# Performance work log

Measured on AMD Instinct MI355X. Metric: run time of the kernel, lower is better.

Reference implementation:

```python
import jax, jax.numpy as jnp
import numpy as np

SEQ_LEN, BATCH, N_FEATURES, CONTEXT = 2048, 32, 1024, 20


def setup_inputs() -> dict:
    key = jax.random.key(0)
    k1, k2 = jax.random.split(key)
    x = jax.random.normal(k1, (SEQ_LEN, BATCH, N_FEATURES), dtype=jnp.float32)
    stdv = 1.0 / np.sqrt(CONTEXT + 1)
    weight = jax.random.uniform(
        k2, (N_FEATURES, CONTEXT + 1), dtype=jnp.float32, minval=-stdv, maxval=stdv
    )
    return {"x": x, "weight": weight}


def reference(x, weight):
    # x: (S, B, F); weight: (F, C+1)
    # y[t, b, f] = sum_{c=0}^{C} x[t+c, b, f] * weight[f, c], zero-padded past t=S-1.
    S, B, F = x.shape
    C = weight.shape[1] - 1
    lhs = jnp.transpose(x, (1, 2, 0))          # (B, F, S)  NCW layout
    rhs = weight[:, None, :]                   # (F, 1, C+1) depthwise kernel
    out = jax.lax.conv_general_dilated(
        lhs, rhs,
        window_strides=(1,),
        padding=[(0, C)],                      # causal lookahead: pad right only
        feature_group_count=F,
    )                                          # (B, F, S) cross-correlation == torch math
    return jnp.transpose(out, (2, 0, 1))       # (S, B, F)
```

## Files before the change

### kernel.cpp

```cpp
#include <hip/hip_runtime.h>

#define S_LEN   2048
#define BATCH   32
#define NF      1024
#define CTX     20
#define KW      21
#define T_OUT   256
#define F_TILE  32
#define NCHUNK  36
#define BUF_FLOATS (NCHUNK * 8 * F_TILE)
#define R_PER_T 8
#define T_WIN   (R_PER_T + CTX)
#define N_TILES (S_LEN / T_OUT)

#define WAITV(n) asm volatile("s_waitcnt vmcnt(" #n ")" ::: "memory")

typedef float f32x4_t __attribute__((ext_vector_type(4)));

__device__ __forceinline__ void stage_tile(const float* __restrict__ x,
                                           float* buf, int t0_s, int b,
                                           int f0, int wv_id, int rsub, int f4l) {
    #pragma unroll
    for (int j = 0; j < 9; ++j) {
        int chunk = j * 4 + wv_id;
        int row   = chunk * 8 + rsub;
        int t     = t0_s + row;
        t = (t < S_LEN) ? t : (S_LEN - 1);
        const float* src = x + ((size_t)t * BATCH + b) * NF + f0 + (f4l << 2);
        __builtin_amdgcn_global_load_lds(
            (const __attribute__((address_space(1))) void*)src,
            (__attribute__((address_space(3))) void*)(buf + chunk * 256),
            16, 0, 0);
    }
}

__global__ __launch_bounds__(256)
void lookahead_dwconv_kernel(const float* __restrict__ x,
                             const float* __restrict__ w,
                             float* __restrict__ out) {
    __shared__ float xlds[2][BUF_FLOATS];

    const int tid    = threadIdx.x;
    const int f_tile = blockIdx.x;
    const int b      = blockIdx.y;
    const int f0     = f_tile * F_TILE;

    const int wv_id = tid >> 6;
    const int lane  = tid & 63;
    const int rsub  = lane >> 3;
    const int f4l   = lane & 7;

    const int f4    = tid & 7;
    const int tg    = tid >> 3;
    const int tbase = tg * R_PER_T;

    float wv[4][KW];
    {
        const float* wp = w + (size_t)(f0 + f4 * 4) * KW;
        #pragma unroll
        for (int c = 0; c < 4; ++c)
            #pragma unroll
            for (int k = 0; k < KW; ++k)
                wv[c][k] = wp[c * KW + k];
    }

    stage_tile(x, xlds[0], 0, b, f0, wv_id, rsub, f4l);

    #pragma unroll 1
    for (int t_tile = 0; t_tile < N_TILES; ++t_tile) {
        const int cur = t_tile & 1;
        const int t0  = t_tile * T_OUT;

        if (t_tile < N_TILES - 1)
            stage_tile(x, xlds[cur ^ 1], t0 + T_OUT, b, f0, wv_id, rsub, f4l);

        if (t_tile == 0)                 WAITV(9);
        else if (t_tile < N_TILES - 1)   WAITV(17);
        else                             WAITV(8);
        __builtin_amdgcn_s_barrier();

        const float* bp = xlds[cur];

        float4 acc[R_PER_T];
        #pragma unroll
        for (int r = 0; r < R_PER_T; ++r)
            acc[r] = make_float4(0.f, 0.f, 0.f, 0.f);

        if (t_tile < N_TILES - 1) {
            #pragma unroll
            for (int s = 0; s < T_WIN; ++s) {
                const int row = tbase + s;
                float4 xv = *reinterpret_cast<const float4*>(
                    &bp[row * F_TILE + (f4 << 2)]);
                #pragma unroll
                for (int r = 0; r < R_PER_T; ++r) {
                    const int k = s - r;
                    if (k >= 0 && k < KW) {
                        acc[r].x = fmaf(xv.x, wv[0][k], acc[r].x);
                        acc[r].y = fmaf(xv.y, wv[1][k], acc[r].y);
                        acc[r].z = fmaf(xv.z, wv[2][k], acc[r].z);
                        acc[r].w = fmaf(xv.w, wv[3][k], acc[r].w);
                    }
                }
            }
        } else {
            #pragma unroll
            for (int s = 0; s < T_WIN; ++s) {
                const int row = tbase + s;
                float4 xv = *reinterpret_cast<const float4*>(
                    &bp[row * F_TILE + (f4 << 2)]);
                if (t0 + row >= S_LEN) xv = make_float4(0.f, 0.f, 0.f, 0.f);
                #pragma unroll
                for (int r = 0; r < R_PER_T; ++r) {
                    const int k = s - r;
                    if (k >= 0 && k < KW) {
                        acc[r].x = fmaf(xv.x, wv[0][k], acc[r].x);
                        acc[r].y = fmaf(xv.y, wv[1][k], acc[r].y);
                        acc[r].z = fmaf(xv.z, wv[2][k], acc[r].z);
                        acc[r].w = fmaf(xv.w, wv[3][k], acc[r].w);
                    }
                }
            }
        }

        __builtin_amdgcn_s_barrier();

        size_t obase = ((size_t)(t0 + tbase) * BATCH + b) * NF + f0 + (f4 << 2);
        #pragma unroll
        for (int r = 0; r < R_PER_T; ++r) {
            f32x4_t v = { acc[r].x, acc[r].y, acc[r].z, acc[r].w };
            __builtin_nontemporal_store(v,
                reinterpret_cast<f32x4_t*>(&out[obase + (size_t)r * BATCH * NF]));
        }
    }
}

extern "C" void kernel_launch(void* const* d_in, const int* in_sizes, int n_in,
                              void* d_out, int out_size, void* d_ws, size_t ws_size,
                              hipStream_t stream) {
    const float* x = (const float*)d_in[0];
    const float* w = (const float*)d_in[1];
    float* out     = (float*)d_out;

    dim3 grid(NF / F_TILE, BATCH);
    dim3 block(256);
    lookahead_dwconv_kernel<<<grid, block, 0, stream>>>(x, w, out);
}
```

Baseline: 91.23 us.

## Replace halo-duplicating double buffer with three-slab LDS ring

```diff
diff --git a/kernel.cpp b/kernel.cpp
--- a/kernel.cpp
+++ b/kernel.cpp
@@ -5,23 +5,22 @@
 #define NF      1024
 #define CTX     20
 #define KW      21
-#define T_OUT   256
+#define T_OUT   128
 #define F_TILE  32
-#define NCHUNK  36
-#define BUF_FLOATS (NCHUNK * 8 * F_TILE)
-#define R_PER_T 8
+#define R_PER_T 4
 #define T_WIN   (R_PER_T + CTX)
 #define N_TILES (S_LEN / T_OUT)
+#define STAGE_FLOATS 4096
 
 #define WAITV(n) asm volatile("s_waitcnt vmcnt(" #n ")" ::: "memory")
 
 typedef float f32x4_t __attribute__((ext_vector_type(4)));
 
-__device__ __forceinline__ void stage_tile(const float* __restrict__ x,
-                                           float* buf, int t0_s, int b,
+__device__ __forceinline__ void stage_slab(const float* __restrict__ x,
+                                           float* ring, int oDst, int t0_s, int b,
                                            int f0, int wv_id, int rsub, int f4l) {
     #pragma unroll
-    for (int j = 0; j < 9; ++j) {
+    for (int j = 0; j < 4; ++j) {
         int chunk = j * 4 + wv_id;
         int row   = chunk * 8 + rsub;
         int t     = t0_s + row;
@@ -29,7 +28,7 @@
         const float* src = x + ((size_t)t * BATCH + b) * NF + f0 + (f4l << 2);
         __builtin_amdgcn_global_load_lds(
             (const __attribute__((address_space(1))) void*)src,
-            (__attribute__((address_space(3))) void*)(buf + chunk * 256),
+            (__attribute__((address_space(3))) void*)(ring + oDst + chunk * 256),
             16, 0, 0);
     }
 }
@@ -38,7 +37,7 @@
 void lookahead_dwconv_kernel(const float* __restrict__ x,
                              const float* __restrict__ w,
                              float* __restrict__ out) {
-    __shared__ float xlds[2][BUF_FLOATS];
+    __shared__ float ring[3 * STAGE_FLOATS];
 
     const int tid    = threadIdx.x;
     const int f_tile = blockIdx.x;
@@ -64,22 +63,22 @@
                 wv[c][k] = wp[c * KW + k];
     }
 
-    stage_tile(x, xlds[0], 0, b, f0, wv_id, rsub, f4l);
+    stage_slab(x, ring, 0,            0,     b, f0, wv_id, rsub, f4l);
+    stage_slab(x, ring, STAGE_FLOATS, T_OUT, b, f0, wv_id, rsub, f4l);
+
+    int oA = 0, oB = STAGE_FLOATS, oC = 2 * STAGE_FLOATS;
 
     #pragma unroll 1
     for (int t_tile = 0; t_tile < N_TILES; ++t_tile) {
-        const int cur = t_tile & 1;
-        const int t0  = t_tile * T_OUT;
+        const int t0 = t_tile * T_OUT;
 
         if (t_tile < N_TILES - 1)
-            stage_tile(x, xlds[cur ^ 1], t0 + T_OUT, b, f0, wv_id, rsub, f4l);
+            stage_slab(x, ring, oC, t0 + 2 * T_OUT, b, f0, wv_id, rsub, f4l);
 
-        if (t_tile == 0)                 WAITV(9);
-        else if (t_tile < N_TILES - 1)   WAITV(17);
-        else                             WAITV(8);
+        if (t_tile == 0)                 WAITV(4);
+        else if (t_tile < N_TILES - 1)   WAITV(8);
+        else                             WAITV(4);
         __builtin_amdgcn_s_barrier();
-
-        const float* bp = xlds[cur];
 
         float4 acc[R_PER_T];
         #pragma unroll
@@ -90,8 +89,9 @@
             #pragma unroll
             for (int s = 0; s < T_WIN; ++s) {
                 const int row = tbase + s;
-                float4 xv = *reinterpret_cast<const float4*>(
-                    &bp[row * F_TILE + (f4 << 2)]);
+                const int off = (row < T_OUT ? oA : oB - T_OUT * F_TILE)
+                                + row * F_TILE + (f4 << 2);
+                float4 xv = *reinterpret_cast<const float4*>(&ring[off]);
                 #pragma unroll
                 for (int r = 0; r < R_PER_T; ++r) {
                     const int k = s - r;
@@ -107,8 +107,9 @@
             #pragma unroll
             for (int s = 0; s < T_WIN; ++s) {
                 const int row = tbase + s;
-                float4 xv = *reinterpret_cast<const float4*>(
-                    &bp[row * F_TILE + (f4 << 2)]);
+                const int off = (row < T_OUT ? oA : oB - T_OUT * F_TILE)
+                                + row * F_TILE + (f4 << 2);
+                float4 xv = *reinterpret_cast<const float4*>(&ring[off]);
                 if (t0 + row >= S_LEN) xv = make_float4(0.f, 0.f, 0.f, 0.f);
                 #pragma unroll
                 for (int r = 0; r < R_PER_T; ++r) {
@@ -132,6 +133,8 @@
             __builtin_nontemporal_store(v,
                 reinterpret_cast<f32x4_t*>(&out[obase + (size_t)r * BATCH * NF]));
         }
+
+        int tmp = oA; oA = oB; oB = oC; oC = tmp;
     }
 }
 
```

New measurement: 116.2 us. +27.3%, slower.
